# Kernel tuning notes

Measured on AMD Instinct MI355X. Metric: run time of the kernel, lower is better.

Reference implementation:

```python
import jax, jax.numpy as jnp
import numpy as np

DIM = 192
HEADS = 6
WS = (4, 4, 4)
N = 64          # prod(WS)
NW = 64         # windows per sample
BATCH = 2048    # num_windows * B
CPB_HIDDEN = 512


def _make_rpb_tables():
    space = len(WS)
    coords = [np.arange(-(w - 1), w, dtype=np.float32) for w in WS]
    rpb = np.stack(np.meshgrid(*coords, indexing='ij'))  # (3, 7,7,7)
    for i in range(space):
        rpb[i] = rpb[i] / (WS[i] - 1)
    rpb = np.moveaxis(rpb, 0, -1)[None]  # (1,7,7,7,3)
    rpb = 8.0 * rpb
    rpb = np.sign(rpb) * np.log2(np.abs(rpb) + 1.0) / np.log2(8.0)
    grid = np.stack(np.meshgrid(*[np.arange(w) for w in WS], indexing='ij')).reshape(space, -1)  # (3, N)
    dists = grid[:, :, None] - grid[:, None, :]  # (3, N, N)
    for i in range(space):
        center = max(int(np.prod([2 * w - 1 for w in WS[i + 1:]])), 1)
        dists[i] = (dists[i] + WS[i] - 1) * center
    rpb_idx = dists.sum(0)  # (N, N), values in [0, 343)
    return jnp.asarray(rpb, jnp.float32), jnp.asarray(rpb_idx, jnp.int32)


def setup_inputs() -> dict:
    key = jax.random.key(0)
    ks = jax.random.split(key, 8)
    rpb, rpb_idx = _make_rpb_tables()
    s = 0.02
    return {
        'x': jax.random.normal(ks[0], (BATCH, N, DIM), jnp.float32),
        'mask': jnp.zeros((NW, N, N), jnp.float32),
        'rpb': rpb,
        'rpb_idx': rpb_idx,
        'cpb_w1': jax.random.normal(ks[1], (CPB_HIDDEN, len(WS)), jnp.float32) * s,
        'cpb_b1': jnp.zeros((CPB_HIDDEN,), jnp.float32),
        'cpb_w2': jax.random.normal(ks[2], (HEADS, CPB_HIDDEN), jnp.float32) * s,
        'qkv_w': jax.random.normal(ks[3], (3 * DIM, DIM), jnp.float32) * s,
        'qkv_b': jnp.zeros((3 * DIM,), jnp.float32),
        'proj_w': jax.random.normal(ks[4], (DIM, DIM), jnp.float32) * s,
        'proj_b': jnp.zeros((DIM,), jnp.float32),
        'logit_scale': jnp.log(10.0 * jnp.ones((HEADS, 1, 1), jnp.float32)),
    }


def reference(x, mask, rpb, rpb_idx, cpb_w1, cpb_b1, cpb_w2, qkv_w, qkv_b,
              proj_w, proj_b, logit_scale):
    B, n, C = x.shape
    H = logit_scale.shape[0]
    hd = C // H
    # qkv projection -> (3, B, H, n, hd)
    qkv = (x @ qkv_w.T + qkv_b).reshape(B, n, 3, H, hd).transpose(2, 0, 3, 1, 4)
    q, k, v = qkv[0], qkv[1], qkv[2]
    # continuous position bias MLP: (1,7,7,7,3) -> (1,7,7,7,H) -> gather -> (1,H,n,n)
    h1 = jax.nn.relu(rpb @ cpb_w1.T + cpb_b1)
    bias = (h1 @ cpb_w2.T).reshape(-1, H)            # (343, H)
    bias = bias[rpb_idx.reshape(-1)].reshape(n, n, H)
    bias = 16.0 * jax.nn.sigmoid(bias)
    bias = bias.transpose(2, 0, 1)[None]             # (1, H, n, n)
    # cosine attention
    qn = q / jnp.maximum(jnp.linalg.norm(q, axis=-1, keepdims=True), 1e-12)
    kn = k / jnp.maximum(jnp.linalg.norm(k, axis=-1, keepdims=True), 1e-12)
    scale = jnp.exp(jnp.minimum(logit_scale, jnp.log(jnp.float32(100.0))))  # clamp max=log(1/0.01)
    attn = jnp.einsum('bhnd,bhmd->bhnm', qn, kn) * scale + bias
    nW = mask.shape[0]
    attn = attn + jnp.tile(mask[:, None, :, :], (B // nW, 1, 1, 1))  # (B,1,n,n) broadcast over heads
    attn = jax.nn.softmax(attn, axis=-1)
    out = jnp.einsum('bhnm,bhmd->bhnd', attn, v)
    out = out.transpose(0, 2, 1, 3).reshape(B, n, C)  # heads-major concat (b n (h c))
    return out @ proj_w.T + proj_b
```

## Files before the change

kernel.cpp:

```cpp
#include <hip/hip_runtime.h>
#include <hip/hip_bf16.h>

#define DIM 192
#define HEADS 6
#define HD 32
#define NTOK 64
#define BATCH 2048
#define CPBH 512
#define TBL 343
#define NW 64

typedef unsigned int u32;
typedef __attribute__((ext_vector_type(8))) short b16x8;
typedef __attribute__((ext_vector_type(4))) float f32x4;

__device__ __forceinline__ unsigned short f2bf(float f) {
  union { __hip_bfloat16 h; unsigned short s; } cv;
  cv.h = __float2bfloat16(f);
  return cv.s;
}
__device__ __forceinline__ u32 pack2(float a, float b) {
  return (u32)f2bf(a) | ((u32)f2bf(b) << 16);
}
union FragU { u32 u[4]; b16x8 s; uint4 q; };

__device__ __forceinline__ b16x8 ld_frag_g(const u32* p) {
  FragU f; f.q = *(const uint4*)p; return f.s;
}

__global__ __launch_bounds__(256) void k_prep(
    const float* __restrict__ rpb, const float* __restrict__ w1,
    const float* __restrict__ b1, const float* __restrict__ w2,
    float* __restrict__ tab,
    const float* __restrict__ qkvw, const float* __restrict__ pw,
    u32* __restrict__ wq, u32* __restrict__ wp) {
  const int tid = threadIdx.x;
  if (blockIdx.x < 88) {
    int t = blockIdx.x * 4 + (tid >> 6);
    int lane = tid & 63;
    if (t >= TBL) return;
    float r0 = rpb[t*3], r1 = rpb[t*3+1], r2 = rpb[t*3+2];
    float a[HEADS];
    #pragma unroll
    for (int h = 0; h < HEADS; ++h) a[h] = 0.f;
    #pragma unroll
    for (int kk = 0; kk < 8; ++kk) {
      int k = lane * 8 + kk;
      float hv = fmaf(r0, w1[k*3], fmaf(r1, w1[k*3+1], fmaf(r2, w1[k*3+2], b1[k])));
      hv = fmaxf(hv, 0.f);
      #pragma unroll
      for (int h = 0; h < HEADS; ++h) a[h] = fmaf(hv, w2[h*CPBH + k], a[h]);
    }
    #pragma unroll
    for (int h = 0; h < HEADS; ++h) {
      a[h] += __shfl_xor(a[h], 1);  a[h] += __shfl_xor(a[h], 2);
      a[h] += __shfl_xor(a[h], 4);  a[h] += __shfl_xor(a[h], 8);
      a[h] += __shfl_xor(a[h], 16); a[h] += __shfl_xor(a[h], 32);
    }
    if (lane == 0) {
      #pragma unroll
      for (int h = 0; h < HEADS; ++h) tab[t*HEADS + h] = a[h];
    }
    return;
  }
  int i = (blockIdx.x - 88) * 256 + tid;
  if (i < 55296) {
    int R = i / 96, c = i % 96;
    int h  = R / 96;
    int t  = R - h * 96;
    int s3 = t >> 5;
    int u  = t & 31;
    int hf = (u >> 4) & 1;
    int p  = u & 15;
    int d  = ((p >> 2) << 3) + (hf << 2) + (p & 3);
    int orig = s3 * 192 + h * 32 + d;
    wq[i] = pack2(qkvw[orig*192 + 2*c], qkvw[orig*192 + 2*c + 1]);
  } else if (i < 55296 + 18432) {
    int j = i - 55296;
    wp[j] = pack2(pw[2*j], pw[2*j+1]);
  }
}

__global__ void k_bm(const float* __restrict__ tab, const int* __restrict__ ridx,
                     const float* __restrict__ mask, float* __restrict__ bm) {
  int idx = blockIdx.x * blockDim.x + threadIdx.x;
  if (idx >= NW * HEADS * 4096) return;
  int row = idx & 63;
  int col = (idx >> 6) & 63;
  int h = (idx >> 12) % HEADS;
  int nw = idx / (HEADS * 4096);
  int ij = row * 64 + col;
  float v = tab[ridx[ij] * HEADS + h];
  bm[idx] = 16.f / (1.f + __expf(-v)) + mask[nw * 4096 + ij];
}

union RegA { u32 xl[NTOK * 101]; u32 pbt[HEADS][16 * 35]; };
union RegB { u32 vTL[HEADS][32 * 35]; u32 aol[NTOK * 99]; };

__global__ __launch_bounds__(384, 3) void k_fused(
    const float* __restrict__ x, const u32* __restrict__ wq,
    const float* __restrict__ qkvb, const float* __restrict__ bm,
    const float* __restrict__ ls, const u32* __restrict__ wp,
    const float* __restrict__ pb, float* __restrict__ out) {
  __shared__ RegA rA;
  __shared__ RegB rB;

  const int tid = threadIdx.x;
  const int b = blockIdx.x;
  const int h = tid >> 6;
  const int lane = tid & 63;
  const int m = lane & 15, qd = lane >> 4;

  {
    const float4* xg = (const float4*)(x + (size_t)b * (NTOK * DIM));
    for (int i = tid; i < (NTOK * DIM) / 4; i += 384) {
      float4 v = xg[i];
      int flat = i * 4, tok = flat / DIM, k = flat % DIM;
      rA.xl[tok*101 + k/2]     = pack2(v.x, v.y);
      rA.xl[tok*101 + k/2 + 1] = pack2(v.z, v.w);
    }
  }
  __syncthreads();

  b16x8 qfv[4], kfv[4];
  #pragma unroll
  for (int s3 = 0; s3 < 3; ++s3) {
    b16x8 afr[2][6];
    float bv[2][4];
    #pragma unroll
    for (int hf = 0; hf < 2; ++hf) {
      const u32* wrow = wq + (size_t)(((h*3 + s3)*2 + hf)*16 + m) * 96;
      #pragma unroll
      for (int ks = 0; ks < 6; ++ks) afr[hf][ks] = ld_frag_g(wrow + ks*16 + qd*4);
      #pragma unroll
      for (int r = 0; r < 4; ++r) bv[hf][r] = qkvb[s3*192 + h*32 + qd*8 + hf*4 + r];
    }
    #pragma unroll
    for (int t = 0; t < 4; ++t) {
      f32x4 a0 = {0.f,0.f,0.f,0.f}, a1 = {0.f,0.f,0.f,0.f};
      #pragma unroll
      for (int ks = 0; ks < 6; ++ks) {
        b16x8 bfr = *(const b16x8*)(&rA.xl[(t*16 + m)*101 + ks*16 + qd*4]);
        a0 = __builtin_amdgcn_mfma_f32_16x16x32_bf16(afr[0][ks], bfr, a0, 0,0,0);
        a1 = __builtin_amdgcn_mfma_f32_16x16x32_bf16(afr[1][ks], bfr, a1, 0,0,0);
      }
      #pragma unroll
      for (int r = 0; r < 4; ++r) { a0[r] += bv[0][r]; a1[r] += bv[1][r]; }
      if (s3 < 2) {
        float ss = 0.f;
        #pragma unroll
        for (int r = 0; r < 4; ++r) ss = fmaf(a0[r],a0[r], fmaf(a1[r],a1[r], ss));
        ss += __shfl_xor(ss, 16);
        ss += __shfl_xor(ss, 32);
        float inv = 1.f / fmaxf(sqrtf(ss), 1e-12f);
        FragU tf;
        tf.u[0] = pack2(a0[0]*inv, a0[1]*inv);
        tf.u[1] = pack2(a0[2]*inv, a0[3]*inv);
        tf.u[2] = pack2(a1[0]*inv, a1[1]*inv);
        tf.u[3] = pack2(a1[2]*inv, a1[3]*inv);
        if (s3 == 0) qfv[t] = tf.s; else kfv[t] = tf.s;
      } else {
        float v8[8];
        #pragma unroll
        for (int r = 0; r < 4; ++r) { v8[r] = a0[r]; v8[4+r] = a1[r]; }
        #pragma unroll
        for (int e = 0; e < 8; ++e) {
          float pn = __shfl_xor(v8[e], 1);
          if ((m & 1) == 0) {
            int d = qd*8 + (e>>2)*4 + (e&3);
            rB.vTL[h][d*35 + t*8 + (m>>1)] = pack2(v8[e], pn);
          }
        }
      }
    }
  }
  __syncthreads();

  b16x8 vfr[2][2];
  #pragma unroll
  for (int nt = 0; nt < 2; ++nt)
    #pragma unroll
    for (int ks = 0; ks < 2; ++ks)
      vfr[nt][ks] = *(const b16x8*)(&rB.vTL[h][(nt*16 + m)*35 + ks*16 + qd*4]);
  __syncthreads();

  const float sc = __expf(fminf(ls[h], 4.60517019f));
  const float* bmp = bm + ((size_t)(b & 63) * HEADS + h) * 4096;
  u32* pbw = rA.pbt[h];
  #pragma unroll
  for (int mt = 0; mt < 4; ++mt) {
    f32x4 s4[4];
    #pragma unroll
    for (int ct = 0; ct < 4; ++ct) {
      f32x4 z = {0.f,0.f,0.f,0.f};
      s4[ct] = __builtin_amdgcn_mfma_f32_16x16x32_bf16(qfv[mt], kfv[ct], z, 0,0,0);
    }
    #pragma unroll
    for (int ct = 0; ct < 4; ++ct) {
      float4 b4 = *(const float4*)(bmp + (ct*16 + m)*64 + mt*16 + qd*4);
      s4[ct][0] = fmaf(s4[ct][0], sc, b4.x);
      s4[ct][1] = fmaf(s4[ct][1], sc, b4.y);
      s4[ct][2] = fmaf(s4[ct][2], sc, b4.z);
      s4[ct][3] = fmaf(s4[ct][3], sc, b4.w);
    }
    float rinv[4];
    #pragma unroll
    for (int r = 0; r < 4; ++r) {
      float mm = s4[0][r];
      #pragma unroll
      for (int ct = 1; ct < 4; ++ct) mm = fmaxf(mm, s4[ct][r]);
      mm = fmaxf(mm, __shfl_xor(mm, 1)); mm = fmaxf(mm, __shfl_xor(mm, 2));
      mm = fmaxf(mm, __shfl_xor(mm, 4)); mm = fmaxf(mm, __shfl_xor(mm, 8));
      float l = 0.f;
      #pragma unroll
      for (int ct = 0; ct < 4; ++ct) { s4[ct][r] = __expf(s4[ct][r] - mm); l += s4[ct][r]; }
      l += __shfl_xor(l, 1); l += __shfl_xor(l, 2);
      l += __shfl_xor(l, 4); l += __shfl_xor(l, 8);
      rinv[r] = 1.f / l;
      int rloc = qd*4 + r;
      #pragma unroll
      for (int ct = 0; ct < 4; ++ct) {
        float pv = s4[ct][r];
        float pn = __shfl_xor(pv, 1);
        if ((m & 1) == 0) pbw[rloc*35 + ct*8 + (m >> 1)] = pack2(pv, pn);
      }
    }
    b16x8 pa0 = *(const b16x8*)(&pbw[m*35 + qd*4]);
    b16x8 pa1 = *(const b16x8*)(&pbw[m*35 + 16 + qd*4]);
    #pragma unroll
    for (int nt = 0; nt < 2; ++nt) {
      f32x4 o = {0.f,0.f,0.f,0.f};
      o = __builtin_amdgcn_mfma_f32_16x16x32_bf16(pa0, vfr[nt][0], o, 0,0,0);
      o = __builtin_amdgcn_mfma_f32_16x16x32_bf16(pa1, vfr[nt][1], o, 0,0,0);
      #pragma unroll
      for (int r = 0; r < 4; ++r) {
        float val = o[r] * rinv[r];
        float pn = __shfl_xor(val, 1);
        if ((m & 1) == 0)
          rB.aol[(mt*16 + qd*4 + r)*99 + h*16 + nt*8 + (m >> 1)] = pack2(val, pn);
      }
    }
  }
  __syncthreads();

  const int wv = h;
  b16x8 pfr[2][6];
  float pbv[2][4];
  #pragma unroll
  for (int jj = 0; jj < 2; ++jj) {
    const u32* wrow = wp + (size_t)((wv*2 + jj)*16 + m) * 96;
    #pragma unroll
    for (int ks = 0; ks < 6; ++ks) pfr[jj][ks] = ld_frag_g(wrow + ks*16 + qd*4);
    #pragma unroll
    for (int r = 0; r < 4; ++r) pbv[jj][r] = pb[(wv*2 + jj)*16 + qd*4 + r];
  }
  #pragma unroll 1
  for (int t = 0; t < 4; ++t) {
    f32x4 acc0 = {0.f,0.f,0.f,0.f}, acc1 = {0.f,0.f,0.f,0.f};
    #pragma unroll
    for (int ks = 0; ks < 6; ++ks) {
      b16x8 bfr = *(const b16x8*)(&rB.aol[(t*16 + m)*99 + ks*16 + qd*4]);
      acc0 = __builtin_amdgcn_mfma_f32_16x16x32_bf16(pfr[0][ks], bfr, acc0, 0,0,0);
      acc1 = __builtin_amdgcn_mfma_f32_16x16x32_bf16(pfr[1][ks], bfr, acc1, 0,0,0);
    }
    float* op = out + ((size_t)b*64 + t*16 + m) * DIM;
    *(float4*)(op + (wv*2+0)*16 + qd*4) =
        make_float4(acc0[0]+pbv[0][0], acc0[1]+pbv[0][1], acc0[2]+pbv[0][2], acc0[3]+pbv[0][3]);
    *(float4*)(op + (wv*2+1)*16 + qd*4) =
        make_float4(acc1[0]+pbv[1][0], acc1[1]+pbv[1][1], acc1[2]+pbv[1][2], acc1[3]+pbv[1][3]);
  }
}

extern "C" void kernel_launch(void* const* d_in, const int* in_sizes, int n_in,
                              void* d_out, int out_size, void* d_ws, size_t ws_size,
                              hipStream_t stream) {
  const float* x    = (const float*)d_in[0];
  const float* mask = (const float*)d_in[1];
  const float* rpb  = (const float*)d_in[2];
  const int*   ridx = (const int*)d_in[3];
  const float* w1   = (const float*)d_in[4];
  const float* b1   = (const float*)d_in[5];
  const float* w2   = (const float*)d_in[6];
  const float* qkvw = (const float*)d_in[7];
  const float* qkvb = (const float*)d_in[8];
  const float* pw   = (const float*)d_in[9];
  const float* pb   = (const float*)d_in[10];
  const float* ls   = (const float*)d_in[11];
  float* out = (float*)d_out;

  char* ws = (char*)d_ws;
  float* btab = (float*)(ws);
  float* bm   = (float*)(ws + 16384);
  u32* wq = (u32*)(ws + 16384 + 6291456);
  u32* wp = (u32*)(ws + 16384 + 6291456 + 221184);

  k_prep<<<376, 256, 0, stream>>>(rpb, w1, b1, w2, btab, qkvw, pw, wq, wp);
  k_bm<<<(NW * HEADS * 4096 + 255) / 256, 256, 0, stream>>>(btab, ridx, mask, bm);
  k_fused<<<BATCH, 384, 0, stream>>>(x, wq, qkvb, bm, ls, wp, pb, out);
}
```

Before: 446.0 us.

## Transpose score tiles, keep softmax probs in registers, raise occupancy to 8 waves

Computes S^T (K as A operand, Q as B) so each lane owns a full softmax row, and switches the bias-table layout to match. The per-row shuffle reductions become two cross-quad shuffles, and the P fragments are rebuilt through lane permutes instead of an LDS round trip. Weight fragments are now streamed per k-step rather than held, and V stays in LDS instead of registers. Together with the merged LDS union this targets occupancy 8 instead of 3, at the cost of more global weight loads inside the loop and possible register spills.

Result: faster. 408.8 us (-8.3%).

```diff
diff --git a/kernel.cpp b/kernel.cpp
--- a/kernel.cpp
+++ b/kernel.cpp
@@ -26,6 +26,9 @@
 
 __device__ __forceinline__ b16x8 ld_frag_g(const u32* p) {
   FragU f; f.q = *(const uint4*)p; return f.s;
+}
+__device__ __forceinline__ u32 shf(u32 v, int l) {
+  return (u32)__shfl((int)v, l);
 }
 
 __global__ __launch_bounds__(256) void k_prep(
@@ -85,25 +88,22 @@
                      const float* __restrict__ mask, float* __restrict__ bm) {
   int idx = blockIdx.x * blockDim.x + threadIdx.x;
   if (idx >= NW * HEADS * 4096) return;
-  int row = idx & 63;
-  int col = (idx >> 6) & 63;
+  int ij = idx & 4095;
   int h = (idx >> 12) % HEADS;
   int nw = idx / (HEADS * 4096);
-  int ij = row * 64 + col;
   float v = tab[ridx[ij] * HEADS + h];
   bm[idx] = 16.f / (1.f + __expf(-v)) + mask[nw * 4096 + ij];
 }
 
-union RegA { u32 xl[NTOK * 101]; u32 pbt[HEADS][16 * 35]; };
-union RegB { u32 vTL[HEADS][32 * 35]; u32 aol[NTOK * 99]; };
-
-__global__ __launch_bounds__(384, 3) void k_fused(
+union RegA { u32 xl[NTOK * 101]; u32 aol[NTOK * 99]; };
+
+__global__ __launch_bounds__(384, 8) void k_fused(
     const float* __restrict__ x, const u32* __restrict__ wq,
     const float* __restrict__ qkvb, const float* __restrict__ bm,
     const float* __restrict__ ls, const u32* __restrict__ wp,
     const float* __restrict__ pb, float* __restrict__ out) {
   __shared__ RegA rA;
-  __shared__ RegB rB;
+  __shared__ u32 vTL[HEADS][32 * 35];
 
   const int tid = threadIdx.x;
   const int b = blockIdx.x;
@@ -122,31 +122,41 @@
   }
   __syncthreads();
 
-  b16x8 qfv[4], kfv[4];
-  #pragma unroll
-  for (int s3 = 0; s3 < 3; ++s3) {
-    b16x8 afr[2][6];
-    float bv[2][4];
-    #pragma unroll
-    for (int hf = 0; hf < 2; ++hf) {
-      const u32* wrow = wq + (size_t)(((h*3 + s3)*2 + hf)*16 + m) * 96;
-      #pragma unroll
-      for (int ks = 0; ks < 6; ++ks) afr[hf][ks] = ld_frag_g(wrow + ks*16 + qd*4);
-      #pragma unroll
-      for (int r = 0; r < 4; ++r) bv[hf][r] = qkvb[s3*192 + h*32 + qd*8 + hf*4 + r];
-    }
-    #pragma unroll
-    for (int t = 0; t < 4; ++t) {
-      f32x4 a0 = {0.f,0.f,0.f,0.f}, a1 = {0.f,0.f,0.f,0.f};
-      #pragma unroll
+  b16x8 qk[2][4];
+  #pragma unroll
+  for (int s3 = 0; s3 < 2; ++s3) {
+    float bv0[4], bv1[4];
+    #pragma unroll
+    for (int r = 0; r < 4; ++r) {
+      bv0[r] = qkvb[s3*192 + h*32 + qd*8 + r];
+      bv1[r] = qkvb[s3*192 + h*32 + qd*8 + 4 + r];
+    }
+    const u32* w0 = wq + (size_t)(((h*3 + s3)*2 + 0)*16 + m) * 96;
+    const u32* w1 = wq + (size_t)(((h*3 + s3)*2 + 1)*16 + m) * 96;
+    #pragma unroll
+    for (int tp = 0; tp < 2; ++tp) {
+      f32x4 ac[2][2];
+      #pragma unroll
+      for (int tt = 0; tt < 2; ++tt) {
+        ac[tt][0] = (f32x4){0.f,0.f,0.f,0.f};
+        ac[tt][1] = (f32x4){0.f,0.f,0.f,0.f};
+      }
+      #pragma unroll 1
       for (int ks = 0; ks < 6; ++ks) {
-        b16x8 bfr = *(const b16x8*)(&rA.xl[(t*16 + m)*101 + ks*16 + qd*4]);
-        a0 = __builtin_amdgcn_mfma_f32_16x16x32_bf16(afr[0][ks], bfr, a0, 0,0,0);
-        a1 = __builtin_amdgcn_mfma_f32_16x16x32_bf16(afr[1][ks], bfr, a1, 0,0,0);
-      }
-      #pragma unroll
-      for (int r = 0; r < 4; ++r) { a0[r] += bv[0][r]; a1[r] += bv[1][r]; }
-      if (s3 < 2) {
+        b16x8 a0f = ld_frag_g(w0 + ks*16 + qd*4);
+        b16x8 a1f = ld_frag_g(w1 + ks*16 + qd*4);
+        #pragma unroll
+        for (int tt = 0; tt < 2; ++tt) {
+          b16x8 bfr = *(const b16x8*)(&rA.xl[((tp*2+tt)*16 + m)*101 + ks*16 + qd*4]);
+          ac[tt][0] = __builtin_amdgcn_mfma_f32_16x16x32_bf16(a0f, bfr, ac[tt][0], 0,0,0);
+          ac[tt][1] = __builtin_amdgcn_mfma_f32_16x16x32_bf16(a1f, bfr, ac[tt][1], 0,0,0);
+        }
+      }
+      #pragma unroll
+      for (int tt = 0; tt < 2; ++tt) {
+        f32x4 a0 = ac[tt][0], a1 = ac[tt][1];
+        #pragma unroll
+        for (int r = 0; r < 4; ++r) { a0[r] += bv0[r]; a1[r] += bv1[r]; }
         float ss = 0.f;
         #pragma unroll
         for (int r = 0; r < 4; ++r) ss = fmaf(a0[r],a0[r], fmaf(a1[r],a1[r], ss));
@@ -158,116 +168,149 @@
         tf.u[1] = pack2(a0[2]*inv, a0[3]*inv);
         tf.u[2] = pack2(a1[0]*inv, a1[1]*inv);
         tf.u[3] = pack2(a1[2]*inv, a1[3]*inv);
-        if (s3 == 0) qfv[t] = tf.s; else kfv[t] = tf.s;
-      } else {
-        float v8[8];
-        #pragma unroll
-        for (int r = 0; r < 4; ++r) { v8[r] = a0[r]; v8[4+r] = a1[r]; }
-        #pragma unroll
-        for (int e = 0; e < 8; ++e) {
-          float pn = __shfl_xor(v8[e], 1);
-          if ((m & 1) == 0) {
-            int d = qd*8 + (e>>2)*4 + (e&3);
-            rB.vTL[h][d*35 + t*8 + (m>>1)] = pack2(v8[e], pn);
-          }
+        qk[s3][tp*2 + tt] = tf.s;
+      }
+    }
+  }
+  {
+    float bv0[4], bv1[4];
+    #pragma unroll
+    for (int r = 0; r < 4; ++r) {
+      bv0[r] = qkvb[2*192 + h*32 + qd*8 + r];
+      bv1[r] = qkvb[2*192 + h*32 + qd*8 + 4 + r];
+    }
+    const u32* w0 = wq + (size_t)(((h*3 + 2)*2 + 0)*16 + m) * 96;
+    const u32* w1 = wq + (size_t)(((h*3 + 2)*2 + 1)*16 + m) * 96;
+    #pragma unroll 1
+    for (int t = 0; t < 4; ++t) {
+      f32x4 a0 = (f32x4){0.f,0.f,0.f,0.f}, a1 = (f32x4){0.f,0.f,0.f,0.f};
+      #pragma unroll 1
+      for (int ks = 0; ks < 6; ++ks) {
+        b16x8 a0f = ld_frag_g(w0 + ks*16 + qd*4);
+        b16x8 a1f = ld_frag_g(w1 + ks*16 + qd*4);
+        b16x8 bfr = *(const b16x8*)(&rA.xl[(t*16 + m)*101 + ks*16 + qd*4]);
+        a0 = __builtin_amdgcn_mfma_f32_16x16x32_bf16(a0f, bfr, a0, 0,0,0);
+        a1 = __builtin_amdgcn_mfma_f32_16x16x32_bf16(a1f, bfr, a1, 0,0,0);
+      }
+      float v8[8];
+      #pragma unroll
+      for (int r = 0; r < 4; ++r) { v8[r] = a0[r] + bv0[r]; v8[4+r] = a1[r] + bv1[r]; }
+      #pragma unroll
+      for (int e = 0; e < 8; ++e) {
+        float pn = __shfl_xor(v8[e], 1);
+        if ((m & 1) == 0) {
+          int d = qd*8 + (e>>2)*4 + (e&3);
+          vTL[h][d*35 + t*8 + (m>>1)] = pack2(v8[e], pn);
         }
       }
     }
   }
-  __syncthreads();
-
-  b16x8 vfr[2][2];
-  #pragma unroll
-  for (int nt = 0; nt < 2; ++nt)
-    #pragma unroll
-    for (int ks = 0; ks < 2; ++ks)
-      vfr[nt][ks] = *(const b16x8*)(&rB.vTL[h][(nt*16 + m)*35 + ks*16 + qd*4]);
   __syncthreads();
 
   const float sc = __expf(fminf(ls[h], 4.60517019f));
   const float* bmp = bm + ((size_t)(b & 63) * HEADS + h) * 4096;
-  u32* pbw = rA.pbt[h];
+  const int L0 = (((qd*2) & 3) << 4) + m;
+  const int L1 = (((qd*2 + 1) & 3) << 4) + m;
+  const bool lowq = (qd < 2);
   #pragma unroll
   for (int mt = 0; mt < 4; ++mt) {
     f32x4 s4[4];
     #pragma unroll
     for (int ct = 0; ct < 4; ++ct) {
       f32x4 z = {0.f,0.f,0.f,0.f};
-      s4[ct] = __builtin_amdgcn_mfma_f32_16x16x32_bf16(qfv[mt], kfv[ct], z, 0,0,0);
+      s4[ct] = __builtin_amdgcn_mfma_f32_16x16x32_bf16(qk[1][ct], qk[0][mt], z, 0,0,0);
     }
     #pragma unroll
     for (int ct = 0; ct < 4; ++ct) {
-      float4 b4 = *(const float4*)(bmp + (ct*16 + m)*64 + mt*16 + qd*4);
+      float4 b4 = *(const float4*)(bmp + (mt*16 + m)*64 + ct*16 + qd*4);
       s4[ct][0] = fmaf(s4[ct][0], sc, b4.x);
       s4[ct][1] = fmaf(s4[ct][1], sc, b4.y);
       s4[ct][2] = fmaf(s4[ct][2], sc, b4.z);
       s4[ct][3] = fmaf(s4[ct][3], sc, b4.w);
     }
-    float rinv[4];
-    #pragma unroll
-    for (int r = 0; r < 4; ++r) {
-      float mm = s4[0][r];
-      #pragma unroll
-      for (int ct = 1; ct < 4; ++ct) mm = fmaxf(mm, s4[ct][r]);
-      mm = fmaxf(mm, __shfl_xor(mm, 1)); mm = fmaxf(mm, __shfl_xor(mm, 2));
-      mm = fmaxf(mm, __shfl_xor(mm, 4)); mm = fmaxf(mm, __shfl_xor(mm, 8));
-      float l = 0.f;
-      #pragma unroll
-      for (int ct = 0; ct < 4; ++ct) { s4[ct][r] = __expf(s4[ct][r] - mm); l += s4[ct][r]; }
-      l += __shfl_xor(l, 1); l += __shfl_xor(l, 2);
-      l += __shfl_xor(l, 4); l += __shfl_xor(l, 8);
-      rinv[r] = 1.f / l;
-      int rloc = qd*4 + r;
-      #pragma unroll
-      for (int ct = 0; ct < 4; ++ct) {
-        float pv = s4[ct][r];
-        float pn = __shfl_xor(pv, 1);
-        if ((m & 1) == 0) pbw[rloc*35 + ct*8 + (m >> 1)] = pack2(pv, pn);
-      }
-    }
-    b16x8 pa0 = *(const b16x8*)(&pbw[m*35 + qd*4]);
-    b16x8 pa1 = *(const b16x8*)(&pbw[m*35 + 16 + qd*4]);
+    float mm = s4[0][0];
+    #pragma unroll
+    for (int ct = 0; ct < 4; ++ct)
+      #pragma unroll
+      for (int r = 0; r < 4; ++r) mm = fmaxf(mm, s4[ct][r]);
+    mm = fmaxf(mm, __shfl_xor(mm, 16));
+    mm = fmaxf(mm, __shfl_xor(mm, 32));
+    float l = 0.f;
+    #pragma unroll
+    for (int ct = 0; ct < 4; ++ct)
+      #pragma unroll
+      for (int r = 0; r < 4; ++r) { s4[ct][r] = __expf(s4[ct][r] - mm); l += s4[ct][r]; }
+    l += __shfl_xor(l, 16);
+    l += __shfl_xor(l, 32);
+    float rinv = 1.f / l;
+    u32 pk0a = pack2(s4[0][0], s4[0][1]), pk0b = pack2(s4[0][2], s4[0][3]);
+    u32 pk1a = pack2(s4[1][0], s4[1][1]), pk1b = pack2(s4[1][2], s4[1][3]);
+    u32 pk2a = pack2(s4[2][0], s4[2][1]), pk2b = pack2(s4[2][2], s4[2][3]);
+    u32 pk3a = pack2(s4[3][0], s4[3][1]), pk3b = pack2(s4[3][2], s4[3][3]);
+    FragU pa0, pa1;
+    { u32 t0 = shf(pk0a, L0), t1 = shf(pk1a, L0); pa0.u[0] = lowq ? t0 : t1; }
+    { u32 t0 = shf(pk0b, L0), t1 = shf(pk1b, L0); pa0.u[1] = lowq ? t0 : t1; }
+    { u32 t0 = shf(pk0a, L1), t1 = shf(pk1a, L1); pa0.u[2] = lowq ? t0 : t1; }
+    { u32 t0 = shf(pk0b, L1), t1 = shf(pk1b, L1); pa0.u[3] = lowq ? t0 : t1; }
+    { u32 t0 = shf(pk2a, L0), t1 = shf(pk3a, L0); pa1.u[0] = lowq ? t0 : t1; }
+    { u32 t0 = shf(pk2b, L0), t1 = shf(pk3b, L0); pa1.u[1] = lowq ? t0 : t1; }
+    { u32 t0 = shf(pk2a, L1), t1 = shf(pk3a, L1); pa1.u[2] = lowq ? t0 : t1; }
+    { u32 t0 = shf(pk2b, L1), t1 = shf(pk3b, L1); pa1.u[3] = lowq ? t0 : t1; }
+    float rv[4];
+    #pragma unroll
+    for (int r = 0; r < 4; ++r) rv[r] = __shfl(rinv, qd*4 + r);
     #pragma unroll
     for (int nt = 0; nt < 2; ++nt) {
+      b16x8 vf0 = *(const b16x8*)(&vTL[h][(nt*16 + m)*35 + qd*4]);
+      b16x8 vf1 = *(const b16x8*)(&vTL[h][(nt*16 + m)*35 + 16 + qd*4]);
       f32x4 o = {0.f,0.f,0.f,0.f};
-      o = __builtin_amdgcn_mfma_f32_16x16x32_bf16(pa0, vfr[nt][0], o, 0,0,0);
-      o = __builtin_amdgcn_mfma_f32_16x16x32_bf16(pa1, vfr[nt][1], o, 0,0,0);
+      o = __builtin_amdgcn_mfma_f32_16x16x32_bf16(pa0.s, vf0, o, 0,0,0);
+      o = __builtin_amdgcn_mfma_f32_16x16x32_bf16(pa1.s, vf1, o, 0,0,0);
       #pragma unroll
       for (int r = 0; r < 4; ++r) {
-        float val = o[r] * rinv[r];
+        float val = o[r] * rv[r];
         float pn = __shfl_xor(val, 1);
         if ((m & 1) == 0)
-          rB.aol[(mt*16 + qd*4 + r)*99 + h*16 + nt*8 + (m >> 1)] = pack2(val, pn);
+          rA.aol[(mt*16 + qd*4 + r)*99 + h*16 + nt*8 + (m >> 1)] = pack2(val, pn);
       }
     }
   }
   __syncthreads();
 
-  const int wv = h;
-  b16x8 pfr[2][6];
-  float pbv[2][4];
-  #pragma unroll
-  for (int jj = 0; jj < 2; ++jj) {
-    const u32* wrow = wp + (size_t)((wv*2 + jj)*16 + m) * 96;
-    #pragma unroll
-    for (int ks = 0; ks < 6; ++ks) pfr[jj][ks] = ld_frag_g(wrow + ks*16 + qd*4);
-    #pragma unroll
-    for (int r = 0; r < 4; ++r) pbv[jj][r] = pb[(wv*2 + jj)*16 + qd*4 + r];
+  float pbv0[4], pbv1[4];
+  #pragma unroll
+  for (int r = 0; r < 4; ++r) {
+    pbv0[r] = pb[(h*2 + 0)*16 + qd*4 + r];
+    pbv1[r] = pb[(h*2 + 1)*16 + qd*4 + r];
+  }
+  const u32* p0 = wp + (size_t)((h*2 + 0)*16 + m) * 96;
+  const u32* p1 = wp + (size_t)((h*2 + 1)*16 + m) * 96;
+  f32x4 pacc[4][2];
+  #pragma unroll
+  for (int t = 0; t < 4; ++t) {
+    pacc[t][0] = (f32x4){0.f,0.f,0.f,0.f};
+    pacc[t][1] = (f32x4){0.f,0.f,0.f,0.f};
   }
   #pragma unroll 1
+  for (int ks = 0; ks < 6; ++ks) {
+    b16x8 pf0 = ld_frag_g(p0 + ks*16 + qd*4);
+    b16x8 pf1 = ld_frag_g(p1 + ks*16 + qd*4);
+    #pragma unroll
+    for (int t = 0; t < 4; ++t) {
+      b16x8 bfr = *(const b16x8*)(&rA.aol[(t*16 + m)*99 + ks*16 + qd*4]);
+      pacc[t][0] = __builtin_amdgcn_mfma_f32_16x16x32_bf16(pf0, bfr, pacc[t][0], 0,0,0);
+      pacc[t][1] = __builtin_amdgcn_mfma_f32_16x16x32_bf16(pf1, bfr, pacc[t][1], 0,0,0);
+    }
+  }
+  #pragma unroll
   for (int t = 0; t < 4; ++t) {
-    f32x4 acc0 = {0.f,0.f,0.f,0.f}, acc1 = {0.f,0.f,0.f,0.f};
-    #pragma unroll
-    for (int ks = 0; ks < 6; ++ks) {
-      b16x8 bfr = *(const b16x8*)(&rB.aol[(t*16 + m)*99 + ks*16 + qd*4]);
-      acc0 = __builtin_amdgcn_mfma_f32_16x16x32_bf16(pfr[0][ks], bfr, acc0, 0,0,0);
-      acc1 = __builtin_amdgcn_mfma_f32_16x16x32_bf16(pfr[1][ks], bfr, acc1, 0,0,0);
-    }
     float* op = out + ((size_t)b*64 + t*16 + m) * DIM;
-    *(float4*)(op + (wv*2+0)*16 + qd*4) =
-        make_float4(acc0[0]+pbv[0][0], acc0[1]+pbv[0][1], acc0[2]+pbv[0][2], acc0[3]+pbv[0][3]);
-    *(float4*)(op + (wv*2+1)*16 + qd*4) =
-        make_float4(acc1[0]+pbv[1][0], acc1[1]+pbv[1][1], acc1[2]+pbv[1][2], acc1[3]+pbv[1][3]);
+    *(float4*)(op + (h*2+0)*16 + qd*4) =
+        make_float4(pacc[t][0][0]+pbv0[0], pacc[t][0][1]+pbv0[1],
+                    pacc[t][0][2]+pbv0[2], pacc[t][0][3]+pbv0[3]);
+    *(float4*)(op + (h*2+1)*16 + qd*4) =
+        make_float4(pacc[t][1][0]+pbv1[0], pacc[t][1][1]+pbv1[1],
+                    pacc[t][1][2]+pbv1[2], pacc[t][1][3]+pbv1[3]);
   }
 }
 
```
